# Kernel optimization log

Hardware: AMD Instinct MI355X
Metric: run time of the kernel (lower is better)

## Reference

```python
import jax, jax.numpy as jnp
import numpy as np

NUM_JOINTS = 24
NUM_GRAPHS = 65536
# SMPL-like humanoid kinematic tree: parent[i] < i, root has parent -1
PARENT_TREE = np.array([-1, 0, 1, 2, 3, 0, 5, 6, 7, 0, 9, 10, 11, 12, 11,
                        14, 15, 16, 11, 18, 19, 20, 12, 22], dtype=np.int64)


def rotation_6d_to_matrix(d6):
    # standard 6D rotation representation -> 3x3 rotation matrix (rows b1,b2,b3)
    a1, a2 = d6[..., :3], d6[..., 3:]
    b1 = a1 / (jnp.linalg.norm(a1, axis=-1, keepdims=True) + 1e-12)
    a2p = a2 - jnp.sum(b1 * a2, axis=-1, keepdims=True) * b1
    b2 = a2p / (jnp.linalg.norm(a2p, axis=-1, keepdims=True) + 1e-12)
    b3 = jnp.cross(b1, b2)
    return jnp.stack([b1, b2, b3], axis=-2)  # [..., 3, 3]


def setup_inputs() -> dict:
    key = jax.random.key(0)
    k1, k2 = jax.random.split(key)
    B, N = NUM_GRAPHS, NUM_JOINTS
    x = jax.random.normal(k1, (B * N, 6), dtype=jnp.float32)
    offset = jax.random.normal(k2, (B * N, 3), dtype=jnp.float32)
    parent = jnp.tile(jnp.asarray(PARENT_TREE), B)  # [B*N], valid tree per graph
    return {"x": x, "parent": parent, "offset": offset, "num_graphs": B}


def reference(x, parent, offset, num_graphs):
    B = num_graphs
    x = x.reshape(B, -1, x.shape[-1])            # [B, N, 6]
    N = x.shape[1]
    offset = offset.reshape(B, N, 3)             # [B, N, 3]
    parent_np = np.asarray(parent).reshape(B, -1)[0]  # static tree structure

    T = rotation_6d_to_matrix(x)                 # [B, N, 3, 3] local rotations

    pos = [None] * N   # world positions per joint, each [B, 3]
    rot = [None] * N   # world rotations per joint, each [B, 3, 3]
    for i in range(N):  # N is small/static; parent-before-child order
        p = int(parent_np[i])
        if p == -1:
            pos[i] = jnp.zeros((B, 3), dtype=x.dtype)
            rot[i] = T[:, i]
        else:
            pos[i] = jnp.einsum('bij,bj->bi', rot[p], offset[:, i]) + pos[p]
            rot[i] = jnp.einsum('bij,bjk->bik', rot[p], T[:, i])

    positions = jnp.stack(pos, axis=1)           # [B, N, 3]
    return positions.reshape(-1, 3)              # [B*N, 3]
```

## Files before the change

kernel.cpp:

```cpp
#include <hip/hip_runtime.h>
#include <math.h>


#define GPB 64
#define PAD 65

__device__ __forceinline__ void rot6d(float a0, float a1, float a2,
                                      float a3, float a4, float a5,
                                      float T[9]) {
    float n1 = sqrtf(a0*a0 + a1*a1 + a2*a2) + 1e-12f;
    float i1 = 1.0f / n1;
    float b1x = a0*i1, b1y = a1*i1, b1z = a2*i1;
    float d = b1x*a3 + b1y*a4 + b1z*a5;
    float ax = a3 - d*b1x, ay = a4 - d*b1y, az = a5 - d*b1z;
    float n2 = sqrtf(ax*ax + ay*ay + az*az) + 1e-12f;
    float i2 = 1.0f / n2;
    float b2x = ax*i2, b2y = ay*i2, b2z = az*i2;
    T[0] = b1x; T[1] = b1y; T[2] = b1z;
    T[3] = b2x; T[4] = b2y; T[5] = b2z;
    T[6] = b1y*b2z - b1z*b2y;
    T[7] = b1z*b2x - b1x*b2z;
    T[8] = b1x*b2y - b1y*b2x;
}

__device__ __forceinline__ void write_lds(float* xs, float* os_, int t,
                                          const float4 xr[9], const float2 orr[9]) {
#pragma unroll
    for (int k = 0; k < 9; ++k) {
        int i = k * GPB + t;
        int g = i / 9, e = i - g * 9;
        xs[(4*e+0)*PAD + g] = xr[k].x;
        xs[(4*e+1)*PAD + g] = xr[k].y;
        xs[(4*e+2)*PAD + g] = xr[k].z;
        xs[(4*e+3)*PAD + g] = xr[k].w;
        os_[(2*e+0)*PAD + g] = orr[k].x;
        os_[(2*e+1)*PAD + g] = orr[k].y;
    }
}

template<int J>
__device__ __forceinline__ void joint_step(const float* xs, const float* os_,
                                           float* outs, int t,
                                           float R[9], float Pc[3]) {
    constexpr int jl = J % 6;
    float a0 = xs[(jl*6+0)*PAD + t];
    float a1 = xs[(jl*6+1)*PAD + t];
    float a2 = xs[(jl*6+2)*PAD + t];
    float a3 = xs[(jl*6+3)*PAD + t];
    float a4 = xs[(jl*6+4)*PAD + t];
    float a5 = xs[(jl*6+5)*PAD + t];
    float T[9];
    rot6d(a0, a1, a2, a3, a4, a5, T);
    float o0 = os_[(jl*3+0)*PAD + t];
    float o1 = os_[(jl*3+1)*PAD + t];
    float o2 = os_[(jl*3+2)*PAD + t];
    float p0 = R[0]*o0 + R[1]*o1 + R[2]*o2 + Pc[0];
    float p1 = R[3]*o0 + R[4]*o1 + R[5]*o2 + Pc[1];
    float p2 = R[6]*o0 + R[7]*o1 + R[8]*o2 + Pc[2];
    float Rn[9];
#pragma unroll
    for (int i = 0; i < 3; ++i)
#pragma unroll
        for (int k = 0; k < 3; ++k)
            Rn[i*3+k] = R[i*3+0]*T[0+k] + R[i*3+1]*T[3+k] + R[i*3+2]*T[6+k];
#pragma unroll
    for (int i = 0; i < 9; ++i) R[i] = Rn[i];
    Pc[0] = p0; Pc[1] = p1; Pc[2] = p2;
    outs[(J*3+0)*PAD + t] = p0;
    outs[(J*3+1)*PAD + t] = p1;
    outs[(J*3+2)*PAD + t] = p2;
}

template<int H>
__device__ __forceinline__ void flush_half(const float* outs, float4* out4,
                                           long outb4, int t) {
#pragma unroll
    for (int k = 0; k < 9; ++k) {
        int i = k * GPB + t;
        int g = i / 9, e = i - g * 9;
        float4 v;
        v.x = outs[(36*H + 4*e + 0)*PAD + g];
        v.y = outs[(36*H + 4*e + 1)*PAD + g];
        v.z = outs[(36*H + 4*e + 2)*PAD + g];
        v.w = outs[(36*H + 4*e + 3)*PAD + g];
        out4[outb4 + (long)g*18 + 9*H + e] = v;
    }
}

__global__ __launch_bounds__(GPB, 1) void fk_kernel(const float* __restrict__ x,
                                                    const float* __restrict__ off,
                                                    float* __restrict__ out, int B) {
    __shared__ float xs[36 * PAD];
    __shared__ float os_[18 * PAD];
    __shared__ float outs[72 * PAD];
    int t = threadIdx.x;
    long gb0 = (long)blockIdx.x * GPB;
    const float4* x4 = (const float4*)x;
    const float2* o2g = (const float2*)off;
    long xb4 = gb0 * 36;
    long ob2 = gb0 * 36;

    float4 xr[4][9];
    float2 orr[4][9];
#pragma unroll
    for (int c = 0; c < 4; ++c) {
#pragma unroll
        for (int k = 0; k < 9; ++k) {
            int i = k * GPB + t;
            int g = i / 9, e = i - g * 9;
            xr[c][k] = x4[xb4 + (long)g * 36 + c * 9 + e];
        }
#pragma unroll
        for (int k = 0; k < 9; ++k) {
            int i = k * GPB + t;
            int g = i / 9, e = i - g * 9;
            orr[c][k] = o2g[ob2 + (long)g * 36 + c * 9 + e];
        }
    }

    float R[9], Pc[3], R0[9], R11[9], P11[3], R12[9], P12[3];
    float4* out4 = (float4*)out;
    long outb4 = gb0 * 18;

    write_lds(xs, os_, t, xr[0], orr[0]);
    __syncthreads();
    {
        float a0 = xs[0*PAD+t], a1 = xs[1*PAD+t], a2 = xs[2*PAD+t];
        float a3 = xs[3*PAD+t], a4 = xs[4*PAD+t], a5 = xs[5*PAD+t];
        rot6d(a0, a1, a2, a3, a4, a5, R);
        Pc[0] = Pc[1] = Pc[2] = 0.0f;
        outs[0*PAD+t] = 0.0f; outs[1*PAD+t] = 0.0f; outs[2*PAD+t] = 0.0f;
#pragma unroll
        for (int i = 0; i < 9; ++i) R0[i] = R[i];
    }
    joint_step<1>(xs, os_, outs, t, R, Pc);
    joint_step<2>(xs, os_, outs, t, R, Pc);
    joint_step<3>(xs, os_, outs, t, R, Pc);
    joint_step<4>(xs, os_, outs, t, R, Pc);
#pragma unroll
    for (int i = 0; i < 9; ++i) R[i] = R0[i];
    Pc[0] = Pc[1] = Pc[2] = 0.0f;
    joint_step<5>(xs, os_, outs, t, R, Pc);
    __syncthreads();

    write_lds(xs, os_, t, xr[1], orr[1]);
    __syncthreads();
    joint_step<6>(xs, os_, outs, t, R, Pc);
    joint_step<7>(xs, os_, outs, t, R, Pc);
    joint_step<8>(xs, os_, outs, t, R, Pc);
#pragma unroll
    for (int i = 0; i < 9; ++i) R[i] = R0[i];
    Pc[0] = Pc[1] = Pc[2] = 0.0f;
    joint_step<9>(xs, os_, outs, t, R, Pc);
    joint_step<10>(xs, os_, outs, t, R, Pc);
    joint_step<11>(xs, os_, outs, t, R, Pc);
#pragma unroll
    for (int i = 0; i < 9; ++i) R11[i] = R[i];
    P11[0] = Pc[0]; P11[1] = Pc[1]; P11[2] = Pc[2];
    flush_half<0>(outs, out4, outb4, t);
    __syncthreads();

    write_lds(xs, os_, t, xr[2], orr[2]);
    __syncthreads();
    joint_step<12>(xs, os_, outs, t, R, Pc);
#pragma unroll
    for (int i = 0; i < 9; ++i) R12[i] = R[i];
    P12[0] = Pc[0]; P12[1] = Pc[1]; P12[2] = Pc[2];
    joint_step<13>(xs, os_, outs, t, R, Pc);
#pragma unroll
    for (int i = 0; i < 9; ++i) R[i] = R11[i];
    Pc[0] = P11[0]; Pc[1] = P11[1]; Pc[2] = P11[2];
    joint_step<14>(xs, os_, outs, t, R, Pc);
    joint_step<15>(xs, os_, outs, t, R, Pc);
    joint_step<16>(xs, os_, outs, t, R, Pc);
    joint_step<17>(xs, os_, outs, t, R, Pc);
    __syncthreads();

    write_lds(xs, os_, t, xr[3], orr[3]);
    __syncthreads();
#pragma unroll
    for (int i = 0; i < 9; ++i) R[i] = R11[i];
    Pc[0] = P11[0]; Pc[1] = P11[1]; Pc[2] = P11[2];
    joint_step<18>(xs, os_, outs, t, R, Pc);
    joint_step<19>(xs, os_, outs, t, R, Pc);
    joint_step<20>(xs, os_, outs, t, R, Pc);
    joint_step<21>(xs, os_, outs, t, R, Pc);
#pragma unroll
    for (int i = 0; i < 9; ++i) R[i] = R12[i];
    Pc[0] = P12[0]; Pc[1] = P12[1]; Pc[2] = P12[2];
    joint_step<22>(xs, os_, outs, t, R, Pc);
    joint_step<23>(xs, os_, outs, t, R, Pc);
    flush_half<1>(outs, out4, outb4, t);
}

__global__ __launch_bounds__(256) void fk_tail(const float* __restrict__ x,
                                               const float* __restrict__ off,
                                               float* __restrict__ out,
                                               int b0, int B) {
    int b = b0 + blockIdx.x * blockDim.x + threadIdx.x;
    if (b >= B) return;
    const float* xb = x + (size_t)b * 144;
    const float* ob = off + (size_t)b * 72;
    float* P = out + (size_t)b * 72;
    float R[9], Pc[3], R0[9], R11[9], P11[3], R12[9], P12[3];
    {
        rot6d(xb[0], xb[1], xb[2], xb[3], xb[4], xb[5], R);
        Pc[0] = Pc[1] = Pc[2] = 0.0f;
        P[0] = P[1] = P[2] = 0.0f;
        for (int i = 0; i < 9; ++i) R0[i] = R[i];
    }
    for (int j = 1; j < 24; ++j) {
        float Rp[9], Pp[3];
        if (j==1||j==5||j==9) { for (int i=0;i<9;++i) Rp[i]=R0[i]; Pp[0]=Pp[1]=Pp[2]=0.f; }
        else if (j==14||j==18) { for (int i=0;i<9;++i) Rp[i]=R11[i]; Pp[0]=P11[0];Pp[1]=P11[1];Pp[2]=P11[2]; }
        else if (j==22)   { for (int i=0;i<9;++i) Rp[i]=R12[i]; Pp[0]=P12[0];Pp[1]=P12[1];Pp[2]=P12[2]; }
        else              { for (int i=0;i<9;++i) Rp[i]=R[i];   Pp[0]=Pc[0];Pp[1]=Pc[1];Pp[2]=Pc[2]; }
        float T[9];
        rot6d(xb[j*6+0],xb[j*6+1],xb[j*6+2],xb[j*6+3],xb[j*6+4],xb[j*6+5],T);
        float o0=ob[j*3+0],o1=ob[j*3+1],o2=ob[j*3+2];
        Pc[0]=Rp[0]*o0+Rp[1]*o1+Rp[2]*o2+Pp[0];
        Pc[1]=Rp[3]*o0+Rp[4]*o1+Rp[5]*o2+Pp[1];
        Pc[2]=Rp[6]*o0+Rp[7]*o1+Rp[8]*o2+Pp[2];
        for (int i=0;i<3;++i) for (int k=0;k<3;++k) {
            float s=0.f; for (int m=0;m<3;++m) s+=Rp[i*3+m]*T[m*3+k];
            R[i*3+k]=s;
        }
        P[j*3+0]=Pc[0]; P[j*3+1]=Pc[1]; P[j*3+2]=Pc[2];
        if (j==11) { for (int i=0;i<9;++i) R11[i]=R[i]; P11[0]=Pc[0];P11[1]=Pc[1];P11[2]=Pc[2]; }
        if (j==12) { for (int i=0;i<9;++i) R12[i]=R[i]; P12[0]=Pc[0];P12[1]=Pc[1];P12[2]=Pc[2]; }
    }
}

extern "C" void kernel_launch(void* const* d_in, const int* in_sizes, int n_in,
                              void* d_out, int out_size, void* d_ws, size_t ws_size,
                              hipStream_t stream) {
    const float* x   = (const float*)d_in[0];
    const float* off = (const float*)d_in[2];
    float* out = (float*)d_out;
    int B = in_sizes[0] / 144;
    int nb = B / GPB;
    if (nb > 0)
        fk_kernel<<<nb, GPB, 0, stream>>>(x, off, out, B);
    int rem = B - nb * GPB;
    if (rem > 0)
        fk_tail<<<(rem + 255) / 256, 256, 0, stream>>>(x, off, out, nb * GPB, B);
}
```

Before: 24.44 us.

## Split kinematic tree branches across four waves per block sharing LDS

Each block still handles 64 graphs, but now uses 256 threads (four wavefronts) instead of one. Each wave computes a different subtree of the kinematic chain. Branch-point transforms for joints 11 and 12 are handed between waves through a shared LDS arena across a barrier. All inputs are loaded with coalesced float4/float2 reads in one pass, and the output is flushed once at the end. This is meant to raise per-graph parallelism and latency hiding, which were limited by the serial 24-joint chain running on a single wave. The cost is load imbalance between waves (wave 3 waits and then runs eight steps), extra barriers, and heavy register use for the buffered per-joint transforms.

```diff
diff --git a/kernel.cpp b/kernel.cpp
--- a/kernel.cpp
+++ b/kernel.cpp
@@ -2,17 +2,20 @@
 #include <math.h>
 
 
-#define GPB 64
 #define PAD 65
-
-__device__ __forceinline__ void rot6d(float a0, float a1, float a2,
-                                      float a3, float a4, float a5,
-                                      float T[9]) {
-    float n1 = sqrtf(a0*a0 + a1*a1 + a2*a2) + 1e-12f;
+#define G   64
+
+#define XS(f,g)   arena[(f)*PAD + (g)]
+#define OS(f,g)   arena[(144+(f))*PAD + (g)]
+#define OUTS(r,g) arena[(144+(r))*PAD + (g)]
+#define HF(r,g)   arena[(216+(r))*PAD + (g)]
+
+__device__ __forceinline__ void rot6d(const float a[6], float T[9]) {
+    float n1 = sqrtf(a[0]*a[0] + a[1]*a[1] + a[2]*a[2]) + 1e-12f;
     float i1 = 1.0f / n1;
-    float b1x = a0*i1, b1y = a1*i1, b1z = a2*i1;
-    float d = b1x*a3 + b1y*a4 + b1z*a5;
-    float ax = a3 - d*b1x, ay = a4 - d*b1y, az = a5 - d*b1z;
+    float b1x = a[0]*i1, b1y = a[1]*i1, b1z = a[2]*i1;
+    float d = b1x*a[3] + b1y*a[4] + b1z*a[5];
+    float ax = a[3] - d*b1x, ay = a[4] - d*b1y, az = a[5] - d*b1z;
     float n2 = sqrtf(ax*ax + ay*ay + az*az) + 1e-12f;
     float i2 = 1.0f / n2;
     float b2x = ax*i2, b2y = ay*i2, b2z = az*i2;
@@ -23,40 +26,30 @@
     T[8] = b1x*b2y - b1y*b2x;
 }
 
-__device__ __forceinline__ void write_lds(float* xs, float* os_, int t,
-                                          const float4 xr[9], const float2 orr[9]) {
-#pragma unroll
-    for (int k = 0; k < 9; ++k) {
-        int i = k * GPB + t;
-        int g = i / 9, e = i - g * 9;
-        xs[(4*e+0)*PAD + g] = xr[k].x;
-        xs[(4*e+1)*PAD + g] = xr[k].y;
-        xs[(4*e+2)*PAD + g] = xr[k].z;
-        xs[(4*e+3)*PAD + g] = xr[k].w;
-        os_[(2*e+0)*PAD + g] = orr[k].x;
-        os_[(2*e+1)*PAD + g] = orr[k].y;
-    }
-}
-
 template<int J>
-__device__ __forceinline__ void joint_step(const float* xs, const float* os_,
-                                           float* outs, int t,
-                                           float R[9], float Pc[3]) {
-    constexpr int jl = J % 6;
-    float a0 = xs[(jl*6+0)*PAD + t];
-    float a1 = xs[(jl*6+1)*PAD + t];
-    float a2 = xs[(jl*6+2)*PAD + t];
-    float a3 = xs[(jl*6+3)*PAD + t];
-    float a4 = xs[(jl*6+4)*PAD + t];
-    float a5 = xs[(jl*6+5)*PAD + t];
-    float T[9];
-    rot6d(a0, a1, a2, a3, a4, a5, T);
-    float o0 = os_[(jl*3+0)*PAD + t];
-    float o1 = os_[(jl*3+1)*PAD + t];
-    float o2 = os_[(jl*3+2)*PAD + t];
-    float p0 = R[0]*o0 + R[1]*o1 + R[2]*o2 + Pc[0];
-    float p1 = R[3]*o0 + R[4]*o1 + R[5]*o2 + Pc[1];
-    float p2 = R[6]*o0 + R[7]*o1 + R[8]*o2 + Pc[2];
+__device__ __forceinline__ void pullX(const float* arena, int t, float T[9]) {
+    float a[6];
+#pragma unroll
+    for (int c = 0; c < 6; ++c) a[c] = XS(6*J+c, t);
+    rot6d(a, T);
+}
+
+template<int J>
+__device__ __forceinline__ void pull(const float* arena, int t, float T[9], float o[3]) {
+    float a[6];
+#pragma unroll
+    for (int c = 0; c < 6; ++c) a[c] = XS(6*J+c, t);
+#pragma unroll
+    for (int c = 0; c < 3; ++c) o[c] = OS(3*J+c, t);
+    rot6d(a, T);
+}
+
+template<int J>
+__device__ __forceinline__ void chain_step(float* arena, int t, float R[9], float P[3],
+                                           const float T[9], const float o[3]) {
+    float p0 = R[0]*o[0] + R[1]*o[1] + R[2]*o[2] + P[0];
+    float p1 = R[3]*o[0] + R[4]*o[1] + R[5]*o[2] + P[1];
+    float p2 = R[6]*o[0] + R[7]*o[1] + R[8]*o[2] + P[2];
     float Rn[9];
 #pragma unroll
     for (int i = 0; i < 3; ++i)
@@ -65,132 +58,139 @@
             Rn[i*3+k] = R[i*3+0]*T[0+k] + R[i*3+1]*T[3+k] + R[i*3+2]*T[6+k];
 #pragma unroll
     for (int i = 0; i < 9; ++i) R[i] = Rn[i];
-    Pc[0] = p0; Pc[1] = p1; Pc[2] = p2;
-    outs[(J*3+0)*PAD + t] = p0;
-    outs[(J*3+1)*PAD + t] = p1;
-    outs[(J*3+2)*PAD + t] = p2;
-}
-
-template<int H>
-__device__ __forceinline__ void flush_half(const float* outs, float4* out4,
-                                           long outb4, int t) {
+    P[0] = p0; P[1] = p1; P[2] = p2;
+    OUTS(3*J+0, t) = p0; OUTS(3*J+1, t) = p1; OUTS(3*J+2, t) = p2;
+}
+
+__global__ __launch_bounds__(256, 2) void fk_kernel(const float* __restrict__ x,
+                                                    const float* __restrict__ off,
+                                                    float* __restrict__ out) {
+    __shared__ float arena[240 * PAD];
+    const int tid = threadIdx.x;
+    const int w = tid >> 6;
+    const int t = tid & 63;
+    const long gb0 = (long)blockIdx.x * G;
+    const float4* x4 = (const float4*)x;
+    const float2* o2 = (const float2*)off;
+
+    float4 xr[9]; float2 orr[9];
+#pragma unroll
+    for (int k = 0; k < 9; ++k) xr[k]  = x4[gb0*36 + k*256 + tid];
+#pragma unroll
+    for (int k = 0; k < 9; ++k) orr[k] = o2[gb0*36 + k*256 + tid];
 #pragma unroll
     for (int k = 0; k < 9; ++k) {
-        int i = k * GPB + t;
-        int g = i / 9, e = i - g * 9;
-        float4 v;
-        v.x = outs[(36*H + 4*e + 0)*PAD + g];
-        v.y = outs[(36*H + 4*e + 1)*PAD + g];
-        v.z = outs[(36*H + 4*e + 2)*PAD + g];
-        v.w = outs[(36*H + 4*e + 3)*PAD + g];
-        out4[outb4 + (long)g*18 + 9*H + e] = v;
-    }
-}
-
-__global__ __launch_bounds__(GPB, 1) void fk_kernel(const float* __restrict__ x,
-                                                    const float* __restrict__ off,
-                                                    float* __restrict__ out, int B) {
-    __shared__ float xs[36 * PAD];
-    __shared__ float os_[18 * PAD];
-    __shared__ float outs[72 * PAD];
-    int t = threadIdx.x;
-    long gb0 = (long)blockIdx.x * GPB;
-    const float4* x4 = (const float4*)x;
-    const float2* o2g = (const float2*)off;
-    long xb4 = gb0 * 36;
-    long ob2 = gb0 * 36;
-
-    float4 xr[4][9];
-    float2 orr[4][9];
-#pragma unroll
-    for (int c = 0; c < 4; ++c) {
-#pragma unroll
-        for (int k = 0; k < 9; ++k) {
-            int i = k * GPB + t;
-            int g = i / 9, e = i - g * 9;
-            xr[c][k] = x4[xb4 + (long)g * 36 + c * 9 + e];
+        int i = k*256 + tid; int g = i/36, e = i - g*36;
+        XS(4*e+0, g) = xr[k].x; XS(4*e+1, g) = xr[k].y;
+        XS(4*e+2, g) = xr[k].z; XS(4*e+3, g) = xr[k].w;
+    }
+#pragma unroll
+    for (int k = 0; k < 9; ++k) {
+        int i = k*256 + tid; int g = i/36, e = i - g*36;
+        OS(2*e+0, g) = orr[k].x; OS(2*e+1, g) = orr[k].y;
+    }
+    __syncthreads();
+
+    float Ta[8][9], oa[8][3];
+    float R[9], P[3];
+
+    if (w == 0) {
+        pullX<0>(arena, t, R);
+        pull<1>(arena, t, Ta[0], oa[0]);
+        pull<2>(arena, t, Ta[1], oa[1]);
+        pull<3>(arena, t, Ta[2], oa[2]);
+        pull<4>(arena, t, Ta[3], oa[3]);
+        pull<22>(arena, t, Ta[4], oa[4]);
+        pull<23>(arena, t, Ta[5], oa[5]);
+        P[0] = P[1] = P[2] = 0.0f;
+        OUTS(0, t) = 0.0f; OUTS(1, t) = 0.0f; OUTS(2, t) = 0.0f;
+        chain_step<1>(arena, t, R, P, Ta[0], oa[0]);
+        chain_step<2>(arena, t, R, P, Ta[1], oa[1]);
+        chain_step<3>(arena, t, R, P, Ta[2], oa[2]);
+        chain_step<4>(arena, t, R, P, Ta[3], oa[3]);
+    } else if (w == 1) {
+        pullX<0>(arena, t, R);
+        pull<5>(arena, t, Ta[0], oa[0]);
+        pull<6>(arena, t, Ta[1], oa[1]);
+        pull<7>(arena, t, Ta[2], oa[2]);
+        pull<8>(arena, t, Ta[3], oa[3]);
+        P[0] = P[1] = P[2] = 0.0f;
+        chain_step<5>(arena, t, R, P, Ta[0], oa[0]);
+        chain_step<6>(arena, t, R, P, Ta[1], oa[1]);
+        chain_step<7>(arena, t, R, P, Ta[2], oa[2]);
+        chain_step<8>(arena, t, R, P, Ta[3], oa[3]);
+    } else if (w == 2) {
+        pullX<0>(arena, t, R);
+        pull<9> (arena, t, Ta[0], oa[0]);
+        pull<10>(arena, t, Ta[1], oa[1]);
+        pull<11>(arena, t, Ta[2], oa[2]);
+        pull<12>(arena, t, Ta[3], oa[3]);
+        pull<13>(arena, t, Ta[4], oa[4]);
+        P[0] = P[1] = P[2] = 0.0f;
+        chain_step<9> (arena, t, R, P, Ta[0], oa[0]);
+        chain_step<10>(arena, t, R, P, Ta[1], oa[1]);
+        chain_step<11>(arena, t, R, P, Ta[2], oa[2]);
+#pragma unroll
+        for (int i = 0; i < 9; ++i) HF(i, t) = R[i];
+#pragma unroll
+        for (int c = 0; c < 3; ++c) HF(9+c, t) = P[c];
+        chain_step<12>(arena, t, R, P, Ta[3], oa[3]);
+#pragma unroll
+        for (int i = 0; i < 9; ++i) HF(12+i, t) = R[i];
+#pragma unroll
+        for (int c = 0; c < 3; ++c) HF(21+c, t) = P[c];
+        chain_step<13>(arena, t, R, P, Ta[4], oa[4]);
+    } else {
+        pull<14>(arena, t, Ta[0], oa[0]);
+        pull<15>(arena, t, Ta[1], oa[1]);
+        pull<16>(arena, t, Ta[2], oa[2]);
+        pull<17>(arena, t, Ta[3], oa[3]);
+        pull<18>(arena, t, Ta[4], oa[4]);
+        pull<19>(arena, t, Ta[5], oa[5]);
+        pull<20>(arena, t, Ta[6], oa[6]);
+        pull<21>(arena, t, Ta[7], oa[7]);
+    }
+    __syncthreads();
+
+    if (w == 0) {
+#pragma unroll
+        for (int i = 0; i < 9; ++i) R[i] = HF(12+i, t);
+#pragma unroll
+        for (int c = 0; c < 3; ++c) P[c] = HF(21+c, t);
+        chain_step<22>(arena, t, R, P, Ta[4], oa[4]);
+        chain_step<23>(arena, t, R, P, Ta[5], oa[5]);
+    } else if (w == 3) {
+#pragma unroll
+        for (int i = 0; i < 9; ++i) R[i] = HF(i, t);
+#pragma unroll
+        for (int c = 0; c < 3; ++c) P[c] = HF(9+c, t);
+        chain_step<14>(arena, t, R, P, Ta[0], oa[0]);
+        chain_step<15>(arena, t, R, P, Ta[1], oa[1]);
+        chain_step<16>(arena, t, R, P, Ta[2], oa[2]);
+        chain_step<17>(arena, t, R, P, Ta[3], oa[3]);
+#pragma unroll
+        for (int i = 0; i < 9; ++i) R[i] = HF(i, t);
+#pragma unroll
+        for (int c = 0; c < 3; ++c) P[c] = HF(9+c, t);
+        chain_step<18>(arena, t, R, P, Ta[4], oa[4]);
+        chain_step<19>(arena, t, R, P, Ta[5], oa[5]);
+        chain_step<20>(arena, t, R, P, Ta[6], oa[6]);
+        chain_step<21>(arena, t, R, P, Ta[7], oa[7]);
+    }
+    __syncthreads();
+
+    float4* out4 = (float4*)out;
+#pragma unroll
+    for (int k = 0; k < 5; ++k) {
+        int i = k*256 + tid;
+        if (i < 1152) {
+            int g = i/18, e = i - g*18;
+            float4 v;
+            v.x = OUTS(4*e+0, g); v.y = OUTS(4*e+1, g);
+            v.z = OUTS(4*e+2, g); v.w = OUTS(4*e+3, g);
+            out4[gb0*18 + i] = v;
         }
-#pragma unroll
-        for (int k = 0; k < 9; ++k) {
-            int i = k * GPB + t;
-            int g = i / 9, e = i - g * 9;
-            orr[c][k] = o2g[ob2 + (long)g * 36 + c * 9 + e];
-        }
-    }
-
-    float R[9], Pc[3], R0[9], R11[9], P11[3], R12[9], P12[3];
-    float4* out4 = (float4*)out;
-    long outb4 = gb0 * 18;
-
-    write_lds(xs, os_, t, xr[0], orr[0]);
-    __syncthreads();
-    {
-        float a0 = xs[0*PAD+t], a1 = xs[1*PAD+t], a2 = xs[2*PAD+t];
-        float a3 = xs[3*PAD+t], a4 = xs[4*PAD+t], a5 = xs[5*PAD+t];
-        rot6d(a0, a1, a2, a3, a4, a5, R);
-        Pc[0] = Pc[1] = Pc[2] = 0.0f;
-        outs[0*PAD+t] = 0.0f; outs[1*PAD+t] = 0.0f; outs[2*PAD+t] = 0.0f;
-#pragma unroll
-        for (int i = 0; i < 9; ++i) R0[i] = R[i];
-    }
-    joint_step<1>(xs, os_, outs, t, R, Pc);
-    joint_step<2>(xs, os_, outs, t, R, Pc);
-    joint_step<3>(xs, os_, outs, t, R, Pc);
-    joint_step<4>(xs, os_, outs, t, R, Pc);
-#pragma unroll
-    for (int i = 0; i < 9; ++i) R[i] = R0[i];
-    Pc[0] = Pc[1] = Pc[2] = 0.0f;
-    joint_step<5>(xs, os_, outs, t, R, Pc);
-    __syncthreads();
-
-    write_lds(xs, os_, t, xr[1], orr[1]);
-    __syncthreads();
-    joint_step<6>(xs, os_, outs, t, R, Pc);
-    joint_step<7>(xs, os_, outs, t, R, Pc);
-    joint_step<8>(xs, os_, outs, t, R, Pc);
-#pragma unroll
-    for (int i = 0; i < 9; ++i) R[i] = R0[i];
-    Pc[0] = Pc[1] = Pc[2] = 0.0f;
-    joint_step<9>(xs, os_, outs, t, R, Pc);
-    joint_step<10>(xs, os_, outs, t, R, Pc);
-    joint_step<11>(xs, os_, outs, t, R, Pc);
-#pragma unroll
-    for (int i = 0; i < 9; ++i) R11[i] = R[i];
-    P11[0] = Pc[0]; P11[1] = Pc[1]; P11[2] = Pc[2];
-    flush_half<0>(outs, out4, outb4, t);
-    __syncthreads();
-
-    write_lds(xs, os_, t, xr[2], orr[2]);
-    __syncthreads();
-    joint_step<12>(xs, os_, outs, t, R, Pc);
-#pragma unroll
-    for (int i = 0; i < 9; ++i) R12[i] = R[i];
-    P12[0] = Pc[0]; P12[1] = Pc[1]; P12[2] = Pc[2];
-    joint_step<13>(xs, os_, outs, t, R, Pc);
-#pragma unroll
-    for (int i = 0; i < 9; ++i) R[i] = R11[i];
-    Pc[0] = P11[0]; Pc[1] = P11[1]; Pc[2] = P11[2];
-    joint_step<14>(xs, os_, outs, t, R, Pc);
-    joint_step<15>(xs, os_, outs, t, R, Pc);
-    joint_step<16>(xs, os_, outs, t, R, Pc);
-    joint_step<17>(xs, os_, outs, t, R, Pc);
-    __syncthreads();
-
-    write_lds(xs, os_, t, xr[3], orr[3]);
-    __syncthreads();
-#pragma unroll
-    for (int i = 0; i < 9; ++i) R[i] = R11[i];
-    Pc[0] = P11[0]; Pc[1] = P11[1]; Pc[2] = P11[2];
-    joint_step<18>(xs, os_, outs, t, R, Pc);
-    joint_step<19>(xs, os_, outs, t, R, Pc);
-    joint_step<20>(xs, os_, outs, t, R, Pc);
-    joint_step<21>(xs, os_, outs, t, R, Pc);
-#pragma unroll
-    for (int i = 0; i < 9; ++i) R[i] = R12[i];
-    Pc[0] = P12[0]; Pc[1] = P12[1]; Pc[2] = P12[2];
-    joint_step<22>(xs, os_, outs, t, R, Pc);
-    joint_step<23>(xs, os_, outs, t, R, Pc);
-    flush_half<1>(outs, out4, outb4, t);
+    }
 }
 
 __global__ __launch_bounds__(256) void fk_tail(const float* __restrict__ x,
@@ -204,7 +204,8 @@
     float* P = out + (size_t)b * 72;
     float R[9], Pc[3], R0[9], R11[9], P11[3], R12[9], P12[3];
     {
-        rot6d(xb[0], xb[1], xb[2], xb[3], xb[4], xb[5], R);
+        float a[6] = {xb[0],xb[1],xb[2],xb[3],xb[4],xb[5]};
+        rot6d(a, R);
         Pc[0] = Pc[1] = Pc[2] = 0.0f;
         P[0] = P[1] = P[2] = 0.0f;
         for (int i = 0; i < 9; ++i) R0[i] = R[i];
@@ -216,7 +217,8 @@
         else if (j==22)   { for (int i=0;i<9;++i) Rp[i]=R12[i]; Pp[0]=P12[0];Pp[1]=P12[1];Pp[2]=P12[2]; }
         else              { for (int i=0;i<9;++i) Rp[i]=R[i];   Pp[0]=Pc[0];Pp[1]=Pc[1];Pp[2]=Pc[2]; }
         float T[9];
-        rot6d(xb[j*6+0],xb[j*6+1],xb[j*6+2],xb[j*6+3],xb[j*6+4],xb[j*6+5],T);
+        float a[6] = {xb[j*6+0],xb[j*6+1],xb[j*6+2],xb[j*6+3],xb[j*6+4],xb[j*6+5]};
+        rot6d(a, T);
         float o0=ob[j*3+0],o1=ob[j*3+1],o2=ob[j*3+2];
         Pc[0]=Rp[0]*o0+Rp[1]*o1+Rp[2]*o2+Pp[0];
         Pc[1]=Rp[3]*o0+Rp[4]*o1+Rp[5]*o2+Pp[1];
@@ -238,10 +240,10 @@
     const float* off = (const float*)d_in[2];
     float* out = (float*)d_out;
     int B = in_sizes[0] / 144;
-    int nb = B / GPB;
+    int nb = B / G;
     if (nb > 0)
-        fk_kernel<<<nb, GPB, 0, stream>>>(x, off, out, B);
-    int rem = B - nb * GPB;
+        fk_kernel<<<nb, 256, 0, stream>>>(x, off, out);
+    int rem = B - nb * G;
     if (rem > 0)
-        fk_tail<<<(rem + 255) / 256, 256, 0, stream>>>(x, off, out, nb * GPB, B);
-}
+        fk_tail<<<(rem + 255) / 256, 256, 0, stream>>>(x, off, out, nb * G, B);
+}
```

New measurement: 21.56 us. -11.8%, faster.
